# Kernel optimization log

Measured on AMD Instinct MI355X. Metric: run time of the kernel, lower is better.

## Reference

```python
import jax, jax.numpy as jnp
import numpy as np

LN_EPS = 1e-5

def _ln(x, g, b):
    mu = jnp.mean(x, axis=-1, keepdims=True)
    var = jnp.mean((x - mu) ** 2, axis=-1, keepdims=True)
    return (x - mu) * jax.lax.rsqrt(var + LN_EPS) * g + b

def _gelu(x):
    return jax.nn.gelu(x, approximate=False)

def _time_embed(t, dim):
    # standard sinusoidal embedding on scalar times t: (B,) -> (B, dim)
    half = dim // 2
    freqs = jnp.exp(-jnp.log(10000.0) * jnp.arange(half, dtype=jnp.float32) / max(half - 1, 1))
    ang = t[:, None] * freqs[None, :]
    return jnp.concatenate([jnp.sin(ang), jnp.cos(ang)], axis=-1)

def setup_inputs() -> dict:
    key = jax.random.key(0)
    B, D, C, H, M = 1024, 128, 256, 512, 64
    ks = jax.random.split(key, 24)
    w = lambda k, shp: jax.random.normal(k, shp, dtype=jnp.float32) * 0.02
    inp = {
        "noise": jax.random.normal(ks[0], (B, D), dtype=jnp.float32),
        "context": jax.random.normal(ks[1], (B, C), dtype=jnp.float32),
        "support_memory": jax.random.normal(ks[2], (B, M, D), dtype=jnp.float32),
        "num_steps": 4,
        # memory adapter: LayerNorm(D) + Linear(D->H)
        "mem_ln_g": jnp.ones((D,), jnp.float32), "mem_ln_b": jnp.zeros((D,), jnp.float32),
        "Wa": w(ks[3], (D, H)), "ba": jnp.zeros((H,), jnp.float32),
        # attention projections H->H
        "Wq": w(ks[4], (H, H)), "bq": jnp.zeros((H,), jnp.float32),
        "Wk": w(ks[5], (H, H)), "bk": jnp.zeros((H,), jnp.float32),
        "Wv": w(ks[6], (H, H)), "bv": jnp.zeros((H,), jnp.float32),
        "Wo": w(ks[7], (H, H)), "bo": jnp.zeros((H,), jnp.float32),
        # particle proj: LN(D) + Linear(D->H) + GELU + Linear(H->H)
        "pp_ln_g": jnp.ones((D,), jnp.float32), "pp_ln_b": jnp.zeros((D,), jnp.float32),
        "Wp1": w(ks[8], (D, H)), "bp1": jnp.zeros((H,), jnp.float32),
        "Wp2": w(ks[9], (H, H)), "bp2": jnp.zeros((H,), jnp.float32),
        # context proj C->H
        "Wc": w(ks[10], (C, H)), "bc": jnp.zeros((H,), jnp.float32),
        # time proj H->H (on sinusoidal embedding of dim H)
        "Wt": w(ks[11], (H, H)), "bt": jnp.zeros((H,), jnp.float32),
        # fusion head: LN(4H) + Linear(4H->H) + GELU + Linear(H->D)
        "f_ln_g": jnp.ones((4 * H,), jnp.float32), "f_ln_b": jnp.zeros((4 * H,), jnp.float32),
        "Wf1": w(ks[12], (4 * H, H)), "bf1": jnp.zeros((H,), jnp.float32),
        "Wf2": w(ks[13], (H, D)), "bf2": jnp.zeros((D,), jnp.float32),
    }
    return inp

def reference(noise, context, support_memory, num_steps,
              mem_ln_g, mem_ln_b, Wa, ba,
              Wq, bq, Wk, bk, Wv, bv, Wo, bo,
              pp_ln_g, pp_ln_b, Wp1, bp1, Wp2, bp2,
              Wc, bc, Wt, bt,
              f_ln_g, f_ln_b, Wf1, bf1, Wf2, bf2):
    B, D = noise.shape
    H = Wq.shape[0]
    heads = 4
    dh = H // heads
    scale = dh ** -0.5

    # encode support memory once (solver-invariant), like encode_memory()
    enc = _ln(support_memory, mem_ln_g, mem_ln_b) @ Wa + ba            # (B, M, H)
    M = enc.shape[1]
    k_mem = (enc @ Wk + bk).reshape(B, M, heads, dh)                    # (B, M, h, dh)
    v_mem = (enc @ Wv + bv).reshape(B, M, heads, dh)
    ctx_h = context @ Wc + bc                                           # (B, H)

    def velocity(y, t):
        te = _time_embed(t, H) @ Wt + bt                                # (B, H)
        h = _gelu(_ln(y, pp_ln_g, pp_ln_b) @ Wp1 + bp1) @ Wp2 + bp2      # (B, H)
        q = (h @ Wq + bq).reshape(B, heads, dh)
        logits = jnp.einsum('bhd,bmhd->bhm', q, k_mem) * scale
        attn = jax.nn.softmax(logits, axis=-1)
        summ = jnp.einsum('bhm,bmhd->bhd', attn, v_mem).reshape(B, H)
        m = summ @ Wo + bo                                              # (B, H)
        z = jnp.concatenate([h, m, ctx_h, te], axis=-1)                 # (B, 4H)
        return _gelu(_ln(z, f_ln_g, f_ln_b) @ Wf1 + bf1) @ Wf2 + bf2     # (B, D)

    dt = 1.0 / float(num_steps)
    t0s = jnp.arange(num_steps, dtype=jnp.float32) * dt

    def heun_step(y, t0):
        tb0 = jnp.full((B,), t0, dtype=y.dtype)
        k1 = velocity(y, tb0)
        k2 = velocity(y + dt * k1, tb0 + dt)
        return y + 0.5 * dt * (k1 + k2), None

    y_final, _ = jax.lax.scan(heun_step, noise, t0s)
    return y_final
```

## Files before the change

### kernel.cpp

```cpp
#include <hip/hip_runtime.h>
#include <hip/hip_bf16.h>
#include <cstdint>
#include <cstddef>

#define LN_EPS 1e-5f

typedef __attribute__((ext_vector_type(8))) short short8;
typedef __attribute__((ext_vector_type(4))) float f32x4;

__device__ __forceinline__ float gelu_exact(float x) {
  return 0.5f * x * (1.0f + erff(x * 0.70710678118654752440f));
}
__device__ __forceinline__ float bflo(unsigned int x) {
  union { unsigned int i; float f; } v; v.i = x << 16; return v.f;
}
__device__ __forceinline__ float bfhi(unsigned int x) {
  union { unsigned int i; float f; } v; v.i = x & 0xffff0000u; return v.f;
}
__device__ __forceinline__ float bf2f(short s) {
  union { unsigned int i; float f; } v; v.i = ((unsigned int)(unsigned short)s) << 16; return v.f;
}
__device__ __forceinline__ short bf16s(float f) {
  __hip_bfloat16 h = __float2bfloat16(f);
  return *reinterpret_cast<short*>(&h);
}

__global__ __launch_bounds__(256) void ln_bf16_k(const float* __restrict__ X,
                                                 const float* __restrict__ KIN, float a,
                                                 const float* __restrict__ g,
                                                 const float* __restrict__ bb,
                                                 __hip_bfloat16* __restrict__ out, int rows) {
  int row = blockIdx.x * 4 + (threadIdx.x >> 6);
  if (row >= rows) return;
  int l = threadIdx.x & 63;
  size_t base = (size_t)row * 128;
  float x0 = X[base + l], x1 = X[base + l + 64];
  if (KIN) { x0 += a * KIN[base + l]; x1 += a * KIN[base + l + 64]; }
  float s = x0 + x1;
#pragma unroll
  for (int o = 32; o > 0; o >>= 1) s += __shfl_xor(s, o);
  float mu = s * (1.0f / 128.0f);
  float d0 = x0 - mu, d1 = x1 - mu;
  float v = d0 * d0 + d1 * d1;
#pragma unroll
  for (int o = 32; o > 0; o >>= 1) v += __shfl_xor(v, o);
  float rstd = rsqrtf(v * (1.0f / 128.0f) + LN_EPS);
  out[base + l] = __float2bfloat16(d0 * rstd * g[l] + bb[l]);
  out[base + l + 64] = __float2bfloat16(d1 * rstd * g[l + 64] + bb[l + 64]);
}

template <int ROWS, int BN, bool GELU_OUT, bool OUT_BF16>
__global__ __launch_bounds__(ROWS * 4) void gemm_mfma_k(
    const short* __restrict__ A, const short* __restrict__ WT,
    const float* __restrict__ bias, void* __restrict__ Cout,
    int K, int lda, int ldw, int ldc, float alpha,
    int hsA, int hsB, long hsC) {
// ... 27 lines not shown
    for (int i = 0; i < NB; ++i) {
      int c = tid + i * T;
      bR[i] = *(const short8*)(WT + (size_t)(col0 + (c >> 3)) * ldw + k0 + (c & 7) * 8);
    }
  };
  auto storeT = [&](int buf) {
    int c1 = tid + T;
    *(short8*)&As[buf][tid >> 3][(tid & 7) * 8] = aR0;
    *(short8*)&As[buf][c1 >> 3][(c1 & 7) * 8] = aR1;
#pragma unroll
    for (int i = 0; i < NB; ++i) {
      int c = tid + i * T;
      *(short8*)&Bs[buf][c >> 3][(c & 7) * 8] = bR[i];
    }
  };

  loadA(0);
  loadB(0);
  for (int t = 0; t < nt; ++t) {
    int buf = t & 1;
    storeT(buf);
    __syncthreads();
    if (t + 1 < nt) { loadA(t + 1); loadB(t + 1); }
    short8 af0 = *(const short8*)&As[buf][w * 16 + (l & 15)][(l >> 4) * 8];
    short8 af1 = *(const short8*)&As[buf][w * 16 + (l & 15)][(l >> 4) * 8 + 32];
#pragma unroll
    for (int nc = 0; nc < NFRAG; ++nc) {
      short8 bf0 = *(const short8*)&Bs[buf][nc * 16 + (l & 15)][(l >> 4) * 8];
      acc[nc] = __builtin_amdgcn_mfma_f32_16x16x32_bf16(af0, bf0, acc[nc], 0, 0, 0);
      short8 bf1 = *(const short8*)&Bs[buf][nc * 16 + (l & 15)][(l >> 4) * 8 + 32];
      acc[nc] = __builtin_amdgcn_mfma_f32_16x16x32_bf16(af1, bf1, acc[nc], 0, 0, 0);
    }
    __syncthreads();
  }
  const int cr = (l >> 4) * 4;
  const int cc = l & 15;
#pragma unroll
  for (int nc = 0; nc < NFRAG; ++nc) {
    int gc = col0 + nc * 16 + cc;
    float bv = bias ? bias[gc] : 0.0f;
#pragma unroll
    for (int r = 0; r < 4; ++r) {
      int gr = row0 + w * 16 + cr + r;
      float v = acc[nc][r] * alpha + bv;
      if (GELU_OUT) v = gelu_exact(v);
      if (OUT_BF16)
        ((__hip_bfloat16*)Cout)[cOff + (size_t)gr * ldc + gc] = __float2bfloat16(v);
      else
        ((float*)Cout)[cOff + (size_t)gr * ldc + gc] = v;
    }
  }
}

__global__ __launch_bounds__(128) void zgemm2_k(
    const short* __restrict__ hq, const short* __restrict__ mo,
    const float* __restrict__ ctxWg, const float* __restrict__ teWgRow,
    const float* __restrict__ u, const float* __restrict__ cbv,
    const float* __restrict__ murs, const short* __restrict__ WgT,
    short* __restrict__ outC) {
  __shared__ __align__(16) short As[2][32][72];
  __shared__ __align__(16) short Bs[2][32][72];
  const int tid = threadIdx.x;
  const int w = tid >> 6, l = tid & 63;
  const int row0 = blockIdx.y * 32, col0 = blockIdx.x * 32;
  const int rA0 = tid >> 3, rA1 = rA0 + 16, kc = (tid & 7) * 8;
  f32x4 acc[2];
  acc[0] = (f32x4){0.f, 0.f, 0.f, 0.f};
  acc[1] = (f32x4){0.f, 0.f, 0.f, 0.f};
  short8 aR0, aR1;
  short8 bR[2];
  auto loadA = [&](int t) {
    const int k = t * 64 + kc;
    const short* src;
    int stride, koff;
    if (k < 512) { src = hq; stride = 1024; koff = k; }
    else         { src = mo; stride = 512;  koff = k - 512; }
    aR0 = *(const short8*)(src + (size_t)(row0 + rA0) * stride + koff);
    aR1 = *(const short8*)(src + (size_t)(row0 + rA1) * stride + koff);
  };
  auto loadB = [&](int t) {
    int k0 = t * 64;
#pragma unroll
    for (int i = 0; i < 2; ++i) {
      int c = tid + i * 128;
      bR[i] = *(const short8*)(WgT + (size_t)(col0 + (c >> 3)) * 2048 + k0 + (c & 7) * 8);
    }
  };
  auto storeT = [&](int buf) {
    *(short8*)&As[buf][rA0][kc] = aR0;
    *(short8*)&As[buf][rA1][kc] = aR1;
#pragma unroll
    for (int i = 0; i < 2; ++i) {
      int c = tid + i * 128;
      *(short8*)&Bs[buf][c >> 3][(c & 7) * 8] = bR[i];
    }
  };

  loadA(0);
  loadB(0);
  for (int t = 0; t < 16; ++t) {
    int buf = t & 1;
    storeT(buf);
    __syncthreads();
    if (t + 1 < 16) { loadA(t + 1); loadB(t + 1); }
    short8 af0 = *(const short8*)&As[buf][w * 16 + (l & 15)][(l >> 4) * 8];
    short8 af1 = *(const short8*)&As[buf][w * 16 + (l & 15)][(l >> 4) * 8 + 32];
#pragma unroll
    for (int nc = 0; nc < 2; ++nc) {
      short8 bf0 = *(const short8*)&Bs[buf][nc * 16 + (l & 15)][(l >> 4) * 8];
      acc[nc] = __builtin_amdgcn_mfma_f32_16x16x32_bf16(af0, bf0, acc[nc], 0, 0, 0);
      short8 bf1 = *(const short8*)&Bs[buf][nc * 16 + (l & 15)][(l >> 4) * 8 + 32];
      acc[nc] = __builtin_amdgcn_mfma_f32_16x16x32_bf16(af1, bf1, acc[nc], 0, 0, 0);
    }
    __syncthreads();
  }
  const int cr = (l >> 4) * 4, cc = l & 15;
#pragma unroll
  for (int nc = 0; nc < 2; ++nc) {
    int gc = col0 + nc * 16 + cc;
    float uu = u[gc], cb = cbv[gc], tw = teWgRow[gc];
#pragma unroll
    for (int r = 0; r < 4; ++r) {
      int gr = row0 + w * 16 + cr + r;
      float mu = murs[2 * gr], rs = murs[2 * gr + 1];
      float v = rs * (acc[nc][r] + ctxWg[(size_t)gr * 512 + gc] + tw - mu * uu) + cb;
      outC[(size_t)gr * 512 + gc] = bf16s(gelu_exact(v));
    }
  }
}

__global__ __launch_bounds__(256) void zstats_k(const short* __restrict__ hq,
                                                const short* __restrict__ mo,
                                                const float* __restrict__ ctxsums,
                                                const float* __restrict__ teSums2,
                                                float* __restrict__ murs, int rows) {
  int row = blockIdx.x * 4 + (threadIdx.x >> 6);
  if (row >= rows) return;
  int l = threadIdx.x & 63;
  short8 hv = *(const short8*)(hq + (size_t)row * 1024 + l * 8);
  short8 mv = *(const short8*)(mo + (size_t)row * 512 + l * 8);
  float s = 0.f, s2 = 0.f;
#pragma unroll
  for (int j = 0; j < 8; ++j) {
    float fa = bf2f(hv[j]), fb = bf2f(mv[j]);
    s += fa + fb;
    s2 += fa * fa + fb * fb;
  }
#pragma unroll
  for (int o = 32; o > 0; o >>= 1) { s += __shfl_xor(s, o); s2 += __shfl_xor(s2, o); }
  if (l == 0) {
    float S = s + ctxsums[2 * row] + teSums2[0];
    float S2 = s2 + ctxsums[2 * row + 1] + teSums2[1];
    float mu = S * (1.0f / 2048.0f);
    murs[2 * row] = mu;
    murs[2 * row + 1] = rsqrtf(S2 * (1.0f / 2048.0f) - mu * mu + LN_EPS);
  }
}

__global__ __launch_bounds__(256) void rowsum_k(const short* __restrict__ X,
                                                float* __restrict__ sums, int rows) {
  int row = blockIdx.x * 4 + (threadIdx.x >> 6);
  if (row >= rows) return;
  int l = threadIdx.x & 63;
  short8 v = *(const short8*)(X + (size_t)row * 512 + l * 8);
  float s = 0.f, s2 = 0.f;
#pragma unroll
  for (int j = 0; j < 8; ++j) { float f = bf2f(v[j]); s += f; s2 += f * f; }
#pragma unroll
  for (int o = 32; o > 0; o >>= 1) { s += __shfl_xor(s, o); s2 += __shfl_xor(s2, o); }
  if (l == 0) { sums[2 * row] = s; sums[2 * row + 1] = s2; }
}

__global__ __launch_bounds__(512) void vmp_k(const float* __restrict__ va,
                                             const float* __restrict__ vb,
                                             const float* __restrict__ W,
                                             int woff, int hsA,
                                             float* __restrict__ part) {
  const int j = threadIdx.x;
  const int b = blockIdx.x, z = blockIdx.z;
  const float* vaz = va + (size_t)z * hsA;
  float s = 0.f;
#pragma unroll 4
  for (int i = 0; i < 16; ++i) {
    int k = b * 16 + i;
    float c = vaz[k];
    if (vb) c *= vb[k];
    s += c * W[(size_t)(woff + k) * 512 + j];
  }
  part[((size_t)z * gridDim.x + b) * 512 + j] = s;
}

__global__ __launch_bounds__(512) void vmr_k(const float* __restrict__ part,
                                             const float* __restrict__ base, int KB,
                                             float* __restrict__ out, int hsOut) {
  const int j = threadIdx.x;
  const int z = blockIdx.z;
  float s = base ? base[j] : 0.f;
  for (int b = 0; b < KB; ++b) s += part[((size_t)z * KB + b) * 512 + j];
  out[(size_t)z * hsOut + j] = s;
}

__global__ __launch_bounds__(256) void transpose_cast_scale_k(
    const float* __restrict__ W, const float* __restrict__ scale,
    short* __restrict__ WT, int K, int N) {
  __shared__ float tile[64][65];
  int n0 = blockIdx.x * 64, k0 = blockIdx.y * 64;
#pragma unroll
  for (int i = 0; i < 16; ++i) {
    int e = threadIdx.x + i * 256;
    int r = e >> 6, c = e & 63;
    tile[r][c] = W[(size_t)(k0 + r) * N + n0 + c] * scale[k0 + r];
  }
  __syncthreads();
#pragma unroll
  for (int i = 0; i < 16; ++i) {
    int e = threadIdx.x + i * 256;
    int r = e >> 6, c = e & 63;
    WT[(size_t)(n0 + r) * K + k0 + c] = bf16s(tile[c][r]);
  }
}

__global__ __launch_bounds__(256) void gemm_heun_k(
    const short* __restrict__ A, const short* __restrict__ WT,
    const float* __restrict__ bias, const float* __restrict__ yin,
    const float* __restrict__ kaux, float c0, float* __restrict__ outY) {
  __shared__ __align__(16) short As[2][64][72];
  __shared__ __align__(16) short Bs[2][32][72];
  const int tid = threadIdx.x;
  const int w = tid >> 6, l = tid & 63;
  const int row0 = blockIdx.y * 64, col0 = blockIdx.x * 32;
  f32x4 acc[2];
  acc[0] = (f32x4){0.f, 0.f, 0.f, 0.f};
  acc[1] = (f32x4){0.f, 0.f, 0.f, 0.f};
  short8 aR0, aR1, bR;
  auto loadA = [&](int t) {
    int k0 = t * 64;
    int c1 = tid + 256;
    aR0 = *(const short8*)(A + (size_t)(row0 + (tid >> 3)) * 512 + k0 + (tid & 7) * 8);
    aR1 = *(const short8*)(A + (size_t)(row0 + (c1 >> 3)) * 512 + k0 + (c1 & 7) * 8);
  };
  auto loadB = [&](int t) {
    int k0 = t * 64;
    bR = *(const short8*)(WT + (size_t)(col0 + (tid >> 3)) * 512 + k0 + (tid & 7) * 8);
  };
  auto storeT = [&](int buf) {
    int c1 = tid + 256;
    *(short8*)&As[buf][tid >> 3][(tid & 7) * 8] = aR0;
    *(short8*)&As[buf][c1 >> 3][(c1 & 7) * 8] = aR1;
    *(short8*)&Bs[buf][tid >> 3][(tid & 7) * 8] = bR;
  };
  loadA(0);
  loadB(0);
  for (int t = 0; t < 8; ++t) {
    int buf = t & 1;
    storeT(buf);
    __syncthreads();
    if (t + 1 < 8) { loadA(t + 1); loadB(t + 1); }
    short8 af0 = *(const short8*)&As[buf][w * 16 + (l & 15)][(l >> 4) * 8];
    short8 af1 = *(const short8*)&As[buf][w * 16 + (l & 15)][(l >> 4) * 8 + 32];
#pragma unroll
    for (int nc = 0; nc < 2; ++nc) {
      short8 bf0 = *(const short8*)&Bs[buf][nc * 16 + (l & 15)][(l >> 4) * 8];
      acc[nc] = __builtin_amdgcn_mfma_f32_16x16x32_bf16(af0, bf0, acc[nc], 0, 0, 0);
      short8 bf1 = *(const short8*)&Bs[buf][nc * 16 + (l & 15)][(l >> 4) * 8 + 32];
      acc[nc] = __builtin_amdgcn_mfma_f32_16x16x32_bf16(af1, bf1, acc[nc], 0, 0, 0);
    }
    __syncthreads();
  }
  const int cr = (l >> 4) * 4, cc = l & 15;
#pragma unroll
  for (int nc = 0; nc < 2; ++nc) {
    int gc = col0 + nc * 16 + cc;
    float bv = bias[gc];
#pragma unroll
    for (int r = 0; r < 4; ++r) {
      int gr = row0 + w * 16 + cr + r;
      float v = acc[nc][r] + bv;
      size_t idx = (size_t)gr * 128 + gc;
      outY[idx] = yin[idx] + c0 * (kaux[idx] + v);
    }
  }
}

struct TCBatch { const float* src[5]; short* dst[5]; };
__global__ __launch_bounds__(256) void transpose_cast_batch_k(TCBatch p) {
  const float* W = p.src[blockIdx.z];
  short* WT = p.dst[blockIdx.z];
  __shared__ float tile[64][65];
  int n0 = blockIdx.x * 64, k0 = blockIdx.y * 64;
#pragma unroll
  for (int i = 0; i < 16; ++i) {
    int e = threadIdx.x + i * 256;
    int r = e >> 6, c = e & 63;
    tile[r][c] = W[(size_t)(k0 + r) * 512 + n0 + c];
  }
  __syncthreads();
#pragma unroll
  for (int i = 0; i < 16; ++i) {
    int e = threadIdx.x + i * 256;
    int r = e >> 6, c = e & 63;
    WT[(size_t)(n0 + r) * 512 + k0 + c] = bf16s(tile[c][r]);
  }
}

__global__ __launch_bounds__(256) void transpose_cast_k(const float* __restrict__ W,
                                                        short* __restrict__ WT,
                                                        int K, int N) {
  __shared__ float tile[64][65];
  int n0 = blockIdx.x * 64, k0 = blockIdx.y * 64;
#pragma unroll
  for (int i = 0; i < 16; ++i) {
    int e = threadIdx.x + i * 256;
    int r = e >> 6, c = e & 63;
    tile[r][c] = W[(size_t)(k0 + r) * N + n0 + c];
  }
  __syncthreads();
#pragma unroll
  for (int i = 0; i < 16; ++i) {
    int e = threadIdx.x + i * 256;
    int r = e >> 6, c = e & 63;
    WT[(size_t)(n0 + r) * K + k0 + c] = bf16s(tile[c][r]);
  }
}

__global__ void cast_bf16_k(const float* __restrict__ src, short* __restrict__ dst, int n) {
  int i = blockIdx.x * blockDim.x + threadIdx.x;
  if (i < n) dst[i] = bf16s(src[i]);
}

__global__ __launch_bounds__(256) void bqp_k(const float* __restrict__ bhqq,
                                             const short* __restrict__ Wak_bf,
                                             float scale, float* __restrict__ bqp) {
  const int tid = threadIdx.x;
  const int j = blockIdx.x * 32 + (tid >> 3);
  const int h = j >> 7, e = j & 127;
  const int kl = tid & 7;
  float s = 0.f;
  for (int d = kl; d < 128; d += 8)
    s += bhqq[h * 128 + d] * bf2f(Wak_bf[(size_t)e * 512 + h * 128 + d]);
  s += __shfl_xor(s, 1);
  s += __shfl_xor(s, 2);
  s += __shfl_xor(s, 4);
  if (kl == 0) bqp[j] = s * scale;
}

__global__ __launch_bounds__(512) void te_k(const float* __restrict__ Wt,
                                            const float* __restrict__ bt,
                                            float* __restrict__ te,
                                            float* __restrict__ teSums) {
  __shared__ float emb[512];
  __shared__ float red[8];
  const int ci = blockIdx.x;
  const float t = 0.25f * (float)((ci >> 1) + (ci & 1));
  const int j = threadIdx.x;
  if (j < 256) {
    float fr = expf(-9.210340371976184f * (float)j * (1.0f / 255.0f));
    float ang = t * fr;
    emb[j] = sinf(ang);
    emb[j + 256] = cosf(ang);
  }
  __syncthreads();
  float s0 = 0.f, s1 = 0.f, s2 = 0.f, s3 = 0.f;
  for (int k = 0; k < 512; k += 4) {
    s0 += emb[k] * Wt[(size_t)k * 512 + j];
    s1 += emb[k + 1] * Wt[(size_t)(k + 1) * 512 + j];
    s2 += emb[k + 2] * Wt[(size_t)(k + 2) * 512 + j];
    s3 += emb[k + 3] * Wt[(size_t)(k + 3) * 512 + j];
  }
  float val = bt[j] + ((s0 + s1) + (s2 + s3));
  te[(size_t)ci * 512 + j] = val;
  float sv = val, sq = val * val;
#pragma unroll
  for (int o = 32; o > 0; o >>= 1) { sv += __shfl_xor(sv, o); sq += __shfl_xor(sq, o); }
  if ((j & 63) == 0) red[j >> 6] = sv;
  __syncthreads();
  if (j == 0) {
    float tot = 0.f;
    for (int i = 0; i < 8; ++i) tot += red[i];
    teSums[2 * ci] = tot;
  }
  __syncthreads();
  if ((j & 63) == 0) red[j >> 6] = sq;
  __syncthreads();
  if (j == 0) {
    float tot = 0.f;
    for (int i = 0; i < 8; ++i) tot += red[i];
    teSums[2 * ci + 1] = tot;
  }
}

__global__ __launch_bounds__(256) void attn_k(const __hip_bfloat16* __restrict__ hq,
                                              const short* __restrict__ lnsm,
                                              __hip_bfloat16* __restrict__ sctx) {
  const int b = blockIdx.x;
  const int tid = threadIdx.x;
  const int w = tid >> 6, l = tid & 63;
  __shared__ __align__(16) short smt[64 * 128];
  __shared__ float qs[512];
  __shared__ float att[4][64];
  {
    unsigned int u = ((const unsigned int*)(hq + (size_t)b * 1024 + 512))[tid];
    qs[2 * tid] = bflo(u);
    qs[2 * tid + 1] = bfhi(u);
  }
  {
    const int m = tid >> 2;
    const short* src = lnsm + ((size_t)b * 64 + m) * 128;
#pragma unroll
    for (int j = 0; j < 4; ++j) {
      int c = (tid & 3) + 4 * j;
      short8 v = *(const short8*)(src + c * 8);
      *(short8*)&smt[m * 128 + ((c ^ (m & 7)) * 8)] = v;
    }
  }
  __syncthreads();
  const float* qh = qs + w * 128;
  float acc = 0.f;
#pragma unroll
  for (int i = 0; i < 16; ++i) {
    uint4 u = *(const uint4*)&smt[l * 128 + ((i ^ (l & 7)) * 8)];
    const int d = i * 8;
    acc += bflo(u.x) * qh[d + 0] + bfhi(u.x) * qh[d + 1] +
           bflo(u.y) * qh[d + 2] + bfhi(u.y) * qh[d + 3] +
           bflo(u.z) * qh[d + 4] + bfhi(u.z) * qh[d + 5] +
           bflo(u.w) * qh[d + 6] + bfhi(u.w) * qh[d + 7];
  }
  float mx = acc;
#pragma unroll
  for (int o = 32; o > 0; o >>= 1) mx = fmaxf(mx, __shfl_xor(mx, o));
  float e = expf(acc - mx);
  float se = e;
#pragma unroll
  for (int o = 32; o > 0; o >>= 1) se += __shfl_xor(se, o);
  att[w][l] = e / se;
  const int cb = l >> 2, doff = 2 * (l & 3);
  float a0 = 0.f, a1 = 0.f;
#pragma unroll 8
  for (int m = 0; m < 64; ++m) {
    float am = att[w][m];
    unsigned int u = *(const unsigned int*)&smt[m * 128 + ((cb ^ (m & 7)) * 8) + doff];
    a0 += am * bflo(u);
    a1 += am * bfhi(u);
  }
  unsigned int pr = ((unsigned int)(unsigned short)bf16s(a1) << 16) |
                    (unsigned int)(unsigned short)bf16s(a0);
  ((unsigned int*)(sctx + (size_t)b * 512 + w * 128))[l] = pr;
}

extern "C" void kernel_launch(void* const* d_in, const int* in_sizes, int n_in,
                              void* d_out, int out_size, void* d_ws, size_t ws_size,
                              hipStream_t stream) {
  (void)in_sizes; (void)n_in; (void)out_size; (void)ws_size;
  const int B = 1024, Mm = 64;
  const int BMrows = B * Mm;
  const float ATTN_SCALE = 0.08838834764831845f;
  const size_t SL = (size_t)512 * 512;

  const float* noise = (const float*)d_in[0];
  const float* context = (const float*)d_in[1];
  const float* sm = (const float*)d_in[2];
  const float* mem_ln_g = (const float*)d_in[4];
  const float* mem_ln_b = (const float*)d_in[5];
  const float* Wa = (const float*)d_in[6];
  const float* ba = (const float*)d_in[7];
  const float* Wq = (const float*)d_in[8];
  const float* bq = (const float*)d_in[9];
  const float* Wk = (const float*)d_in[10];
  const float* bk = (const float*)d_in[11];
  (void)bk;
  const float* Wv = (const float*)d_in[12];
  const float* bv = (const float*)d_in[13];
  const float* Wo = (const float*)d_in[14];
  const float* bo = (const float*)d_in[15];
  const float* pp_ln_g = (const float*)d_in[16];
  const float* pp_ln_b = (const float*)d_in[17];
  const float* Wp1 = (const float*)d_in[18];
  const float* bp1 = (const float*)d_in[19];
  const float* Wp2 = (const float*)d_in[20];
  const float* bp2 = (const float*)d_in[21];
  const float* Wc = (const float*)d_in[22];
  const float* bc = (const float*)d_in[23];
  const float* Wt = (const float*)d_in[24];
  const float* bt = (const float*)d_in[25];
  const float* f_ln_g = (const float*)d_in[26];
  const float* f_ln_b = (const float*)d_in[27];
  const float* Wf1 = (const float*)d_in[28];
  const float* bf1 = (const float*)d_in[29];
  const float* Wf2 = (const float*)d_in[30];
  const float* bf2 = (const float*)d_in[31];
  float* out = (float*)d_out;

  char* wsb = (char*)d_ws;
  size_t off = 0;
  auto alloc = [&](size_t bytes) -> void* {
    off = (off + 255) & ~(size_t)255;
    void* p = wsb + off;
    off += bytes;
    return p;
  };
// ... 35 lines not shown
  short* yln = (short*)alloc((size_t)B * 128 * 2);
  short* hmid = (short*)alloc((size_t)B * 512 * 2);
  short* hqbuf = (short*)alloc((size_t)B * 1024 * 2);
  short* sctx = (short*)alloc((size_t)B * 512 * 2);
  short* mobuf = (short*)alloc((size_t)B * 512 * 2);
  short* fmid = (short*)alloc((size_t)B * 512 * 2);

  ln_bf16_k<<<BMrows / 4, 256, 0, stream>>>(sm, nullptr, 0.f, mem_ln_g, mem_ln_b,
                                            (__hip_bfloat16*)lnsm, BMrows);
  cast_bf16_k<<<(128 * 512 + 255) / 256, 256, 0, stream>>>(Wa, WaB, 128 * 512);
  cast_bf16_k<<<(512 * 512 + 255) / 256, 256, 0, stream>>>(Wp2, Wp2B, 512 * 512);
  cast_bf16_k<<<(B * 256 + 255) / 256, 256, 0, stream>>>(context, ctxb, B * 256);
  {
    TCBatch p;
    p.src[0] = Wk; p.src[1] = Wv; p.src[2] = Wq; p.src[3] = Wo; p.src[4] = Wp2;
    p.dst[0] = WkT; p.dst[1] = WvT; p.dst[2] = WqT; p.dst[3] = WoT; p.dst[4] = WhqT;
    transpose_cast_batch_k<<<dim3(8, 8, 5), 256, 0, stream>>>(p);
  }
  transpose_cast_k<<<dim3(8, 2), 256, 0, stream>>>(Wp1, Wp1T, 128, 512);
  transpose_cast_k<<<dim3(8, 4), 256, 0, stream>>>(Wc, WcT, 256, 512);
  transpose_cast_scale_k<<<dim3(8, 32), 256, 0, stream>>>(Wf1, f_ln_g, WgT, 2048, 512);
  transpose_cast_k<<<dim3(2, 8), 256, 0, stream>>>(Wf2, Wf2T, 512, 128);
  gemm_mfma_k<64, 64, false, true><<<dim3(8, 2, 2), 256, 0, stream>>>(
      WaB, WkT, nullptr, WakavB, 512, 512, 512, 512, 1.f, 0, (int)SL, 128 * 512);
  gemm_mfma_k<64, 64, false, true><<<dim3(8, 8), 256, 0, stream>>>(
      Wp2B, WqT, nullptr, Wp2q_bf, 512, 512, 512, 512, 1.f, 0, 0, 0);
  gemm_mfma_k<64, 64, false, true><<<dim3(8, 2, 4), 256, 0, stream>>>(
      Wak_bf, Wp2q_bf, nullptr, WhqT + SL, 128, 512, 512, 512, ATTN_SCALE,
      128, 128, 128 * 512);
  gemm_mfma_k<64, 64, false, true><<<dim3(2, 8, 4), 256, 0, stream>>>(
      WoT, Wav_bf, nullptr, WfoldT, 128, 512, 512, 512, 1.f, 128, 128, 128);
  vmp_k<<<dim3(32, 1, 1), 512, 0, stream>>>(bp2, nullptr, Wq, 0, 0, vpart);
  vmr_k<<<dim3(1, 1, 1), 512, 0, stream>>>(vpart, bq, 32, bhqq, 512);
  bqp_k<<<16, 256, 0, stream>>>(bhqq, Wak_bf, ATTN_SCALE, bhq + 512);
  hipMemcpyAsync(bhq, bp2, 512 * 4, hipMemcpyDeviceToDevice, stream);
  vmp_k<<<dim3(32, 1, 1), 512, 0, stream>>>(ba, nullptr, Wv, 0, 0, vpart);
  vmr_k<<<dim3(1, 1, 1), 512, 0, stream>>>(vpart, bv, 32, bav, 512);
  vmp_k<<<dim3(32, 1, 1), 512, 0, stream>>>(bav, nullptr, Wo, 0, 0, vpart);
  vmr_k<<<dim3(1, 1, 1), 512, 0, stream>>>(vpart, bo, 32, bofold, 512);
  gemm_mfma_k<64, 64, false, true><<<dim3(8, 16), 256, 0, stream>>>(
      ctxb, WcT, bc, ctxh, 256, 256, 256, 512, 1.f, 0, 0, 0);
  te_k<<<8, 512, 0, stream>>>(Wt, bt, te_table, teSums);
  vmp_k<<<dim3(128, 1, 1), 512, 0, stream>>>(f_ln_g, nullptr, Wf1, 0, 0, vpart);
  vmr_k<<<dim3(1, 1, 1), 512, 0, stream>>>(vpart, nullptr, 128, uvec, 512);
  vmp_k<<<dim3(128, 1, 1), 512, 0, stream>>>(f_ln_b, nullptr, Wf1, 0, 0, vpart);
  vmr_k<<<dim3(1, 1, 1), 512, 0, stream>>>(vpart, bf1, 128, cbv, 512);
  vmp_k<<<dim3(32, 1, 8), 512, 0, stream>>>(te_table, f_ln_g + 1536, Wf1, 1536, 512, vpart);
  vmr_k<<<dim3(1, 1, 8), 512, 0, stream>>>(vpart, nullptr, 32, teWg, 512);
  gemm_mfma_k<64, 64, false, false><<<dim3(8, 16), 256, 0, stream>>>(
      ctxh, WgT + 1024, nullptr, ctxWg, 512, 512, 2048, 512, 1.f, 0, 0, 0);
  rowsum_k<<<B / 4, 256, 0, stream>>>(ctxh, ctxsums, B);

  const float dt = 0.25f;
  auto chain = [&](const float* ycur, const float* kin, float a, int tidx) {
    ln_bf16_k<<<B / 4, 256, 0, stream>>>(ycur, kin, a, pp_ln_g, pp_ln_b,
                                         (__hip_bfloat16*)yln, B);
    gemm_mfma_k<32, 32, true, true><<<dim3(16, 32), 128, 0, stream>>>(
        yln, Wp1T, bp1, hmid, 128, 128, 128, 512, 1.f, 0, 0, 0);
    gemm_mfma_k<32, 64, false, true><<<dim3(16, 32), 128, 0, stream>>>(
        hmid, WhqT, bhq, hqbuf, 512, 512, 512, 1024, 1.f, 0, 0, 0);
    attn_k<<<B, 256, 0, stream>>>((const __hip_bfloat16*)hqbuf, lnsm,
                                  (__hip_bfloat16*)sctx);
    gemm_mfma_k<32, 32, false, true><<<dim3(16, 32), 128, 0, stream>>>(
        sctx, WfoldT, bofold, mobuf, 512, 512, 512, 512, 1.f, 0, 0, 0);
    zstats_k<<<B / 4, 256, 0, stream>>>(hqbuf, mobuf, ctxsums, teSums + 2 * tidx,
                                        murs, B);
    zgemm2_k<<<dim3(16, 32), 128, 0, stream>>>(
        hqbuf, mobuf, ctxWg, teWg + (size_t)tidx * 512, uvec, cbv, murs, WgT, fmid);
  };

  const float* ycur = noise;
  for (int s = 0; s < 4; ++s) {
    chain(ycur, nullptr, 0.f, 2 * s);
    gemm_mfma_k<32, 32, false, false><<<dim3(4, 32), 128, 0, stream>>>(
        fmid, Wf2T, bf2, k1, 512, 512, 512, 128, 1.f, 0, 0, 0);
    chain(ycur, k1, dt, 2 * s + 1);
    float* ynext = (s == 3) ? out : ybuf;
    gemm_heun_k<<<dim3(4, 16), 256, 0, stream>>>(
        fmid, Wf2T, bf2, ycur, k1, 0.5f * dt, ynext);
    ycur = ybuf;
  }
}
```

Measured before the change: 587.2 us.

## Fuse per-velocity kernel chain into one cooperative persistent kernel with grid syncs

Replaces the sequence of about eight launches per velocity evaluation (LN, four GEMMs, attention, stats, fusion GEMM, output GEMM) with a single cooperative kernel of 256 blocks that moves between stages using grid.sync(). GEMM tiles become 64-row with 256 threads so each block maps to one tile per stage, and attention is handled as four batch rows per block. The aim is to remove launch overhead and inter-kernel gaps. In exchange, only 256 blocks of one wave-size run at a time, which may reduce occupancy and latency hiding, and each grid barrier has its own cost.

```diff
diff --git a/kernel.cpp b/kernel.cpp
--- a/kernel.cpp
+++ b/kernel.cpp
@@ -1,7 +1,10 @@
 #include <hip/hip_runtime.h>
 #include <hip/hip_bf16.h>
+#include <hip/hip_cooperative_groups.h>
 #include <cstdint>
 #include <cstddef>
+
+namespace cg = cooperative_groups;
 
 #define LN_EPS 1e-5f
 
@@ -135,23 +138,105 @@
   }
 }
 
-__global__ __launch_bounds__(128) void zgemm2_k(
+template <int BN, bool GELU_OUT, bool OUT_BF16, int EPI>
+__device__ __forceinline__ void dev_gemm64(
+    const short* __restrict__ A, const short* __restrict__ WT,
+    const float* __restrict__ bias, void* __restrict__ Cout,
+    int K, int lda, int ldw, int ldc, int tileX, int tileY, char* smem,
+    const float* __restrict__ yin, const float* __restrict__ kaux, float c0) {
+  constexpr int NFRAG = BN / 16;
+  constexpr int NB = (BN * 8) / 256;
+  short (*As)[64][72] = (short (*)[64][72])smem;
+  short (*Bs)[BN][72] = (short (*)[BN][72])(smem + 18432);
+  const int tid = threadIdx.x;
+  const int w = tid >> 6, l = tid & 63;
+  const int row0 = tileY * 64, col0 = tileX * BN;
+  f32x4 acc[NFRAG];
+#pragma unroll
+  for (int i = 0; i < NFRAG; ++i) acc[i] = (f32x4){0.f, 0.f, 0.f, 0.f};
+  const int nt = K >> 6;
+  short8 aR0, aR1;
+  short8 bR[NB];
+  auto loadA = [&](int t) {
+    int k0 = t * 64;
+    int c1 = tid + 256;
+    aR0 = *(const short8*)(A + (size_t)(row0 + (tid >> 3)) * lda + k0 + (tid & 7) * 8);
+    aR1 = *(const short8*)(A + (size_t)(row0 + (c1 >> 3)) * lda + k0 + (c1 & 7) * 8);
+  };
+  auto loadB = [&](int t) {
+    int k0 = t * 64;
+#pragma unroll
+    for (int i = 0; i < NB; ++i) {
+      int c = tid + i * 256;
+      bR[i] = *(const short8*)(WT + (size_t)(col0 + (c >> 3)) * ldw + k0 + (c & 7) * 8);
+    }
+  };
+  auto storeT = [&](int buf) {
+    int c1 = tid + 256;
+    *(short8*)&As[buf][tid >> 3][(tid & 7) * 8] = aR0;
+    *(short8*)&As[buf][c1 >> 3][(c1 & 7) * 8] = aR1;
+#pragma unroll
+    for (int i = 0; i < NB; ++i) {
+      int c = tid + i * 256;
+      *(short8*)&Bs[buf][c >> 3][(c & 7) * 8] = bR[i];
+    }
+  };
+  loadA(0);
+  loadB(0);
+  for (int t = 0; t < nt; ++t) {
+    int buf = t & 1;
+    storeT(buf);
+    __syncthreads();
+    if (t + 1 < nt) { loadA(t + 1); loadB(t + 1); }
+    short8 af0 = *(const short8*)&As[buf][w * 16 + (l & 15)][(l >> 4) * 8];
+    short8 af1 = *(const short8*)&As[buf][w * 16 + (l & 15)][(l >> 4) * 8 + 32];
+#pragma unroll
+    for (int nc = 0; nc < NFRAG; ++nc) {
+      short8 bf0 = *(const short8*)&Bs[buf][nc * 16 + (l & 15)][(l >> 4) * 8];
+      acc[nc] = __builtin_amdgcn_mfma_f32_16x16x32_bf16(af0, bf0, acc[nc], 0, 0, 0);
+      short8 bf1 = *(const short8*)&Bs[buf][nc * 16 + (l & 15)][(l >> 4) * 8 + 32];
+      acc[nc] = __builtin_amdgcn_mfma_f32_16x16x32_bf16(af1, bf1, acc[nc], 0, 0, 0);
+    }
+    __syncthreads();
+  }
+  const int cr = (l >> 4) * 4, cc = l & 15;
+#pragma unroll
+  for (int nc = 0; nc < NFRAG; ++nc) {
+    int gc = col0 + nc * 16 + cc;
+    float bv = bias ? bias[gc] : 0.0f;
+#pragma unroll
+    for (int r = 0; r < 4; ++r) {
+      int gr = row0 + w * 16 + cr + r;
+      float v = acc[nc][r] + bv;
+      if (GELU_OUT) v = gelu_exact(v);
+      size_t idx = (size_t)gr * ldc + gc;
+      if (EPI == 2) {
+        ((float*)Cout)[idx] = yin[idx] + c0 * (kaux[idx] + v);
+      } else if (OUT_BF16) {
+        ((__hip_bfloat16*)Cout)[idx] = __float2bfloat16(v);
+      } else {
+        ((float*)Cout)[idx] = v;
+      }
+    }
+  }
+}
+
+__device__ __forceinline__ void dev_zgemm64(
     const short* __restrict__ hq, const short* __restrict__ mo,
     const float* __restrict__ ctxWg, const float* __restrict__ teWgRow,
     const float* __restrict__ u, const float* __restrict__ cbv,
     const float* __restrict__ murs, const short* __restrict__ WgT,
-    short* __restrict__ outC) {
-  __shared__ __align__(16) short As[2][32][72];
-  __shared__ __align__(16) short Bs[2][32][72];
+    short* __restrict__ outC, int tileX, int tileY, char* smem) {
+  short (*As)[64][72] = (short (*)[64][72])smem;
+  short (*Bs)[32][72] = (short (*)[32][72])(smem + 18432);
   const int tid = threadIdx.x;
   const int w = tid >> 6, l = tid & 63;
-  const int row0 = blockIdx.y * 32, col0 = blockIdx.x * 32;
-  const int rA0 = tid >> 3, rA1 = rA0 + 16, kc = (tid & 7) * 8;
+  const int row0 = tileY * 64, col0 = tileX * 32;
+  const int rA0 = tid >> 3, rA1 = rA0 + 32, kc = (tid & 7) * 8;
   f32x4 acc[2];
   acc[0] = (f32x4){0.f, 0.f, 0.f, 0.f};
   acc[1] = (f32x4){0.f, 0.f, 0.f, 0.f};
-  short8 aR0, aR1;
-  short8 bR[2];
+  short8 aR0, aR1, bR;
   auto loadA = [&](int t) {
     const int k = t * 64 + kc;
     const short* src;
@@ -162,23 +247,13 @@
     aR1 = *(const short8*)(src + (size_t)(row0 + rA1) * stride + koff);
   };
   auto loadB = [&](int t) {
-    int k0 = t * 64;
-#pragma unroll
-    for (int i = 0; i < 2; ++i) {
-      int c = tid + i * 128;
-      bR[i] = *(const short8*)(WgT + (size_t)(col0 + (c >> 3)) * 2048 + k0 + (c & 7) * 8);
-    }
+    bR = *(const short8*)(WgT + (size_t)(col0 + (tid >> 3)) * 2048 + t * 64 + kc);
   };
   auto storeT = [&](int buf) {
     *(short8*)&As[buf][rA0][kc] = aR0;
     *(short8*)&As[buf][rA1][kc] = aR1;
-#pragma unroll
-    for (int i = 0; i < 2; ++i) {
-      int c = tid + i * 128;
-      *(short8*)&Bs[buf][c >> 3][(c & 7) * 8] = bR[i];
-    }
-  };
-
+    *(short8*)&Bs[buf][tid >> 3][kc] = bR;
+  };
   loadA(0);
   loadB(0);
   for (int t = 0; t < 16; ++t) {
@@ -212,46 +287,220 @@
   }
 }
 
-__global__ __launch_bounds__(256) void zstats_k(const short* __restrict__ hq,
-                                                const short* __restrict__ mo,
-                                                const float* __restrict__ ctxsums,
-                                                const float* __restrict__ teSums2,
-                                                float* __restrict__ murs, int rows) {
-  int row = blockIdx.x * 4 + (threadIdx.x >> 6);
-  if (row >= rows) return;
-  int l = threadIdx.x & 63;
-  short8 hv = *(const short8*)(hq + (size_t)row * 1024 + l * 8);
-  short8 mv = *(const short8*)(mo + (size_t)row * 512 + l * 8);
-  float s = 0.f, s2 = 0.f;
-#pragma unroll
-  for (int j = 0; j < 8; ++j) {
-    float fa = bf2f(hv[j]), fb = bf2f(mv[j]);
-    s += fa + fb;
-    s2 += fa * fa + fb * fb;
-  }
-#pragma unroll
-  for (int o = 32; o > 0; o >>= 1) { s += __shfl_xor(s, o); s2 += __shfl_xor(s2, o); }
-  if (l == 0) {
-    float S = s + ctxsums[2 * row] + teSums2[0];
-    float S2 = s2 + ctxsums[2 * row + 1] + teSums2[1];
-    float mu = S * (1.0f / 2048.0f);
-    murs[2 * row] = mu;
-    murs[2 * row + 1] = rsqrtf(S2 * (1.0f / 2048.0f) - mu * mu + LN_EPS);
-  }
-}
-
-__global__ __launch_bounds__(256) void rowsum_k(const short* __restrict__ X,
-                                                float* __restrict__ sums, int rows) {
-  int row = blockIdx.x * 4 + (threadIdx.x >> 6);
-  if (row >= rows) return;
-  int l = threadIdx.x & 63;
-  short8 v = *(const short8*)(X + (size_t)row * 512 + l * 8);
-  float s = 0.f, s2 = 0.f;
-#pragma unroll
-  for (int j = 0; j < 8; ++j) { float f = bf2f(v[j]); s += f; s2 += f * f; }
-#pragma unroll
-  for (int o = 32; o > 0; o >>= 1) { s += __shfl_xor(s, o); s2 += __shfl_xor(s2, o); }
-  if (l == 0) { sums[2 * row] = s; sums[2 * row + 1] = s2; }
+__device__ __forceinline__ void dev_attn(const __hip_bfloat16* __restrict__ hq,
+                                         const short* __restrict__ lnsm,
+                                         __hip_bfloat16* __restrict__ sctx,
+                                         int b, char* smem) {
+  short* smt = (short*)smem;
+  float* qs = (float*)(smem + 16384);
+  float (*att)[64] = (float (*)[64])(smem + 18432);
+  const int tid = threadIdx.x;
+  const int w = tid >> 6, l = tid & 63;
+  {
+    unsigned int u = ((const unsigned int*)(hq + (size_t)b * 1024 + 512))[tid];
+    qs[2 * tid] = bflo(u);
+    qs[2 * tid + 1] = bfhi(u);
+  }
+  {
+    const int m = tid >> 2;
+    const short* src = lnsm + ((size_t)b * 64 + m) * 128;
+#pragma unroll
+    for (int j = 0; j < 4; ++j) {
+      int c = (tid & 3) + 4 * j;
+      short8 v = *(const short8*)(src + c * 8);
+      *(short8*)&smt[m * 128 + ((c ^ (m & 7)) * 8)] = v;
+    }
+  }
+  __syncthreads();
+  const float* qh = qs + w * 128;
+  float acc = 0.f;
+#pragma unroll
+  for (int i = 0; i < 16; ++i) {
+    uint4 u = *(const uint4*)&smt[l * 128 + ((i ^ (l & 7)) * 8)];
+    const int d = i * 8;
+    acc += bflo(u.x) * qh[d + 0] + bfhi(u.x) * qh[d + 1] +
+           bflo(u.y) * qh[d + 2] + bfhi(u.y) * qh[d + 3] +
+           bflo(u.z) * qh[d + 4] + bfhi(u.z) * qh[d + 5] +
+           bflo(u.w) * qh[d + 6] + bfhi(u.w) * qh[d + 7];
+  }
+  float mx = acc;
+#pragma unroll
+  for (int o = 32; o > 0; o >>= 1) mx = fmaxf(mx, __shfl_xor(mx, o));
+  float e = expf(acc - mx);
+  float se = e;
+#pragma unroll
+  for (int o = 32; o > 0; o >>= 1) se += __shfl_xor(se, o);
+  att[w][l] = e / se;
+  const int cb = l >> 2, doff = 2 * (l & 3);
+  float a0 = 0.f, a1 = 0.f;
+#pragma unroll 8
+  for (int m = 0; m < 64; ++m) {
+    float am = att[w][m];
+    unsigned int u = *(const unsigned int*)&smt[m * 128 + ((cb ^ (m & 7)) * 8) + doff];
+    a0 += am * bflo(u);
+    a1 += am * bfhi(u);
+  }
+  unsigned int pr = ((unsigned int)(unsigned short)bf16s(a1) << 16) |
+                    (unsigned int)(unsigned short)bf16s(a0);
+  ((unsigned int*)(sctx + (size_t)b * 512 + w * 128))[l] = pr;
+}
+
+struct SolverArgs {
+  const float* ycur; const float* kin; float a;
+  const float* ppg; const float* ppb; short* yln;
+  const short* Wp1T; const float* bp1; short* hmid;
+  const short* WhqT; const float* bhq; short* hqbuf;
+  const short* lnsm; short* sctx;
+  const short* WfoldT; const float* bofold; short* mobuf;
+  const float* ctxsums; const float* teSums2; float* murs;
+  const short* WgT; const float* ctxWg; const float* teWgRow;
+  const float* uvec; const float* cbv; short* fmid;
+  const short* Wf2T; const float* bf2;
+  float* outY; const float* yin; const float* kaux; float c0;
+};
+
+template <int EPI>
+__global__ __launch_bounds__(256) void solver_k(SolverArgs p) {
+  __shared__ __align__(16) char smem[36864];
+  cg::grid_group grid = cg::this_grid();
+  const int blk = blockIdx.x;
+  const int tid = threadIdx.x;
+
+  {
+    int row = blk * 4 + (tid >> 6);
+    int l = tid & 63;
+    size_t base = (size_t)row * 128;
+    float x0 = p.ycur[base + l], x1 = p.ycur[base + l + 64];
+    if (EPI == 2) { x0 += p.a * p.kin[base + l]; x1 += p.a * p.kin[base + l + 64]; }
+    float s = x0 + x1;
+#pragma unroll
+    for (int o = 32; o > 0; o >>= 1) s += __shfl_xor(s, o);
+    float mu = s * (1.0f / 128.0f);
+    float d0 = x0 - mu, d1 = x1 - mu;
+    float v = d0 * d0 + d1 * d1;
+#pragma unroll
+    for (int o = 32; o > 0; o >>= 1) v += __shfl_xor(v, o);
+    float rstd = rsqrtf(v * (1.0f / 128.0f) + LN_EPS);
+    p.yln[base + l] = bf16s(d0 * rstd * p.ppg[l] + p.ppb[l]);
+    p.yln[base + l + 64] = bf16s(d1 * rstd * p.ppg[l + 64] + p.ppb[l + 64]);
+  }
+  grid.sync();
+  dev_gemm64<32, true, true, 0>(p.yln, p.Wp1T, p.bp1, p.hmid, 128, 128, 128, 512,
+                                blk & 15, blk >> 4, smem, nullptr, nullptr, 0.f);
+  grid.sync();
+  dev_gemm64<64, false, true, 0>(p.hmid, p.WhqT, p.bhq, p.hqbuf, 512, 512, 512, 1024,
+                                 blk & 15, blk >> 4, smem, nullptr, nullptr, 0.f);
+  grid.sync();
+  for (int i = 0; i < 4; ++i) {
+    dev_attn((const __hip_bfloat16*)p.hqbuf, p.lnsm, (__hip_bfloat16*)p.sctx,
+             blk * 4 + i, smem);
+    __syncthreads();
+  }
+  grid.sync();
+  dev_gemm64<32, false, true, 0>(p.sctx, p.WfoldT, p.bofold, p.mobuf, 512, 512, 512, 512,
+                                 blk & 15, blk >> 4, smem, nullptr, nullptr, 0.f);
+  grid.sync();
+  {
+    int row = blk * 4 + (tid >> 6);
+    int l = tid & 63;
+    short8 hv = *(const short8*)(p.hqbuf + (size_t)row * 1024 + l * 8);
+    short8 mv = *(const short8*)(p.mobuf + (size_t)row * 512 + l * 8);
+    float s = 0.f, s2 = 0.f;
+#pragma unroll
+    for (int j = 0; j < 8; ++j) {
+      float fa = bf2f(hv[j]), fb = bf2f(mv[j]);
+      s += fa + fb;
+      s2 += fa * fa + fb * fb;
+    }
+#pragma unroll
+    for (int o = 32; o > 0; o >>= 1) { s += __shfl_xor(s, o); s2 += __shfl_xor(s2, o); }
+    if (l == 0) {
+      float S = s + p.ctxsums[2 * row] + p.teSums2[0];
+      float S2 = s2 + p.ctxsums[2 * row + 1] + p.teSums2[1];
+      float mu = S * (1.0f / 2048.0f);
+      p.murs[2 * row] = mu;
+      p.murs[2 * row + 1] = rsqrtf(S2 * (1.0f / 2048.0f) - mu * mu + LN_EPS);
+    }
+  }
+  grid.sync();
+  dev_zgemm64(p.hqbuf, p.mobuf, p.ctxWg, p.teWgRow, p.uvec, p.cbv, p.murs, p.WgT,
+              p.fmid, blk & 15, blk >> 4, smem);
+  grid.sync();
+  if (blk < 64) {
+    if (EPI == 1) {
+      dev_gemm64<32, false, false, 0>(p.fmid, p.Wf2T, p.bf2, p.outY, 512, 512, 512, 128,
+                                      blk & 3, blk >> 2, smem, nullptr, nullptr, 0.f);
+    } else {
+      dev_gemm64<32, false, false, 2>(p.fmid, p.Wf2T, p.bf2, p.outY, 512, 512, 512, 128,
+                                      blk & 3, blk >> 2, smem, p.yin, p.kaux, p.c0);
+    }
+  }
+}
+
+struct TCBatch { const float* src[5]; short* dst[5]; };
+__global__ __launch_bounds__(256) void transpose_cast_batch_k(TCBatch p) {
+  const float* W = p.src[blockIdx.z];
+  short* WT = p.dst[blockIdx.z];
+  __shared__ float tile[64][65];
+  int n0 = blockIdx.x * 64, k0 = blockIdx.y * 64;
+#pragma unroll
+  for (int i = 0; i < 16; ++i) {
+    int e = threadIdx.x + i * 256;
+    int r = e >> 6, c = e & 63;
+    tile[r][c] = W[(size_t)(k0 + r) * 512 + n0 + c];
+  }
+  __syncthreads();
+#pragma unroll
+  for (int i = 0; i < 16; ++i) {
+    int e = threadIdx.x + i * 256;
+    int r = e >> 6, c = e & 63;
+    WT[(size_t)(n0 + r) * 512 + k0 + c] = bf16s(tile[c][r]);
+  }
+}
+
+__global__ __launch_bounds__(256) void transpose_cast_k(const float* __restrict__ W,
+                                                        short* __restrict__ WT,
+                                                        int K, int N) {
+  __shared__ float tile[64][65];
+  int n0 = blockIdx.x * 64, k0 = blockIdx.y * 64;
+#pragma unroll
+  for (int i = 0; i < 16; ++i) {
+    int e = threadIdx.x + i * 256;
+    int r = e >> 6, c = e & 63;
+    tile[r][c] = W[(size_t)(k0 + r) * N + n0 + c];
+  }
+  __syncthreads();
+#pragma unroll
+  for (int i = 0; i < 16; ++i) {
+    int e = threadIdx.x + i * 256;
+    int r = e >> 6, c = e & 63;
+    WT[(size_t)(n0 + r) * K + k0 + c] = bf16s(tile[c][r]);
+  }
+}
+
+__global__ __launch_bounds__(256) void transpose_cast_scale_k(
+    const float* __restrict__ W, const float* __restrict__ scale,
+    short* __restrict__ WT, int K, int N) {
+  __shared__ float tile[64][65];
+  int n0 = blockIdx.x * 64, k0 = blockIdx.y * 64;
+#pragma unroll
+  for (int i = 0; i < 16; ++i) {
+    int e = threadIdx.x + i * 256;
+    int r = e >> 6, c = e & 63;
+    tile[r][c] = W[(size_t)(k0 + r) * N + n0 + c] * scale[k0 + r];
+  }
+  __syncthreads();
+#pragma unroll
+  for (int i = 0; i < 16; ++i) {
+    int e = threadIdx.x + i * 256;
+    int r = e >> 6, c = e & 63;
+    WT[(size_t)(n0 + r) * K + k0 + c] = bf16s(tile[c][r]);
+  }
+}
+
+__global__ void cast_bf16_k(const float* __restrict__ src, short* __restrict__ dst, int n) {
+  int i = blockIdx.x * blockDim.x + threadIdx.x;
+  if (i < n) dst[i] = bf16s(src[i]);
 }
 
 __global__ __launch_bounds__(512) void vmp_k(const float* __restrict__ va,
@@ -283,134 +532,6 @@
   out[(size_t)z * hsOut + j] = s;
 }
 
-__global__ __launch_bounds__(256) void transpose_cast_scale_k(
-    const float* __restrict__ W, const float* __restrict__ scale,
-    short* __restrict__ WT, int K, int N) {
-  __shared__ float tile[64][65];
-  int n0 = blockIdx.x * 64, k0 = blockIdx.y * 64;
-#pragma unroll
-  for (int i = 0; i < 16; ++i) {
-    int e = threadIdx.x + i * 256;
-    int r = e >> 6, c = e & 63;
-    tile[r][c] = W[(size_t)(k0 + r) * N + n0 + c] * scale[k0 + r];
-  }
-  __syncthreads();
-#pragma unroll
-  for (int i = 0; i < 16; ++i) {
-    int e = threadIdx.x + i * 256;
-    int r = e >> 6, c = e & 63;
-    WT[(size_t)(n0 + r) * K + k0 + c] = bf16s(tile[c][r]);
-  }
-}
-
-__global__ __launch_bounds__(256) void gemm_heun_k(
-    const short* __restrict__ A, const short* __restrict__ WT,
-    const float* __restrict__ bias, const float* __restrict__ yin,
-    const float* __restrict__ kaux, float c0, float* __restrict__ outY) {
-  __shared__ __align__(16) short As[2][64][72];
-  __shared__ __align__(16) short Bs[2][32][72];
-  const int tid = threadIdx.x;
-  const int w = tid >> 6, l = tid & 63;
-  const int row0 = blockIdx.y * 64, col0 = blockIdx.x * 32;
-  f32x4 acc[2];
-  acc[0] = (f32x4){0.f, 0.f, 0.f, 0.f};
-  acc[1] = (f32x4){0.f, 0.f, 0.f, 0.f};
-  short8 aR0, aR1, bR;
-  auto loadA = [&](int t) {
-    int k0 = t * 64;
-    int c1 = tid + 256;
-    aR0 = *(const short8*)(A + (size_t)(row0 + (tid >> 3)) * 512 + k0 + (tid & 7) * 8);
-    aR1 = *(const short8*)(A + (size_t)(row0 + (c1 >> 3)) * 512 + k0 + (c1 & 7) * 8);
-  };
-  auto loadB = [&](int t) {
-    int k0 = t * 64;
-    bR = *(const short8*)(WT + (size_t)(col0 + (tid >> 3)) * 512 + k0 + (tid & 7) * 8);
-  };
-  auto storeT = [&](int buf) {
-    int c1 = tid + 256;
-    *(short8*)&As[buf][tid >> 3][(tid & 7) * 8] = aR0;
-    *(short8*)&As[buf][c1 >> 3][(c1 & 7) * 8] = aR1;
-    *(short8*)&Bs[buf][tid >> 3][(tid & 7) * 8] = bR;
-  };
-  loadA(0);
-  loadB(0);
-  for (int t = 0; t < 8; ++t) {
-    int buf = t & 1;
-    storeT(buf);
-    __syncthreads();
-    if (t + 1 < 8) { loadA(t + 1); loadB(t + 1); }
-    short8 af0 = *(const short8*)&As[buf][w * 16 + (l & 15)][(l >> 4) * 8];
-    short8 af1 = *(const short8*)&As[buf][w * 16 + (l & 15)][(l >> 4) * 8 + 32];
-#pragma unroll
-    for (int nc = 0; nc < 2; ++nc) {
-      short8 bf0 = *(const short8*)&Bs[buf][nc * 16 + (l & 15)][(l >> 4) * 8];
-      acc[nc] = __builtin_amdgcn_mfma_f32_16x16x32_bf16(af0, bf0, acc[nc], 0, 0, 0);
-      short8 bf1 = *(const short8*)&Bs[buf][nc * 16 + (l & 15)][(l >> 4) * 8 + 32];
-      acc[nc] = __builtin_amdgcn_mfma_f32_16x16x32_bf16(af1, bf1, acc[nc], 0, 0, 0);
-    }
-    __syncthreads();
-  }
-  const int cr = (l >> 4) * 4, cc = l & 15;
-#pragma unroll
-  for (int nc = 0; nc < 2; ++nc) {
-    int gc = col0 + nc * 16 + cc;
-    float bv = bias[gc];
-#pragma unroll
-    for (int r = 0; r < 4; ++r) {
-      int gr = row0 + w * 16 + cr + r;
-      float v = acc[nc][r] + bv;
-      size_t idx = (size_t)gr * 128 + gc;
-      outY[idx] = yin[idx] + c0 * (kaux[idx] + v);
-    }
-  }
-}
-
-struct TCBatch { const float* src[5]; short* dst[5]; };
-__global__ __launch_bounds__(256) void transpose_cast_batch_k(TCBatch p) {
-  const float* W = p.src[blockIdx.z];
-  short* WT = p.dst[blockIdx.z];
-  __shared__ float tile[64][65];
-  int n0 = blockIdx.x * 64, k0 = blockIdx.y * 64;
-#pragma unroll
-  for (int i = 0; i < 16; ++i) {
-    int e = threadIdx.x + i * 256;
-    int r = e >> 6, c = e & 63;
-    tile[r][c] = W[(size_t)(k0 + r) * 512 + n0 + c];
-  }
-  __syncthreads();
-#pragma unroll
-  for (int i = 0; i < 16; ++i) {
-    int e = threadIdx.x + i * 256;
-    int r = e >> 6, c = e & 63;
-    WT[(size_t)(n0 + r) * 512 + k0 + c] = bf16s(tile[c][r]);
-  }
-}
-
-__global__ __launch_bounds__(256) void transpose_cast_k(const float* __restrict__ W,
-                                                        short* __restrict__ WT,
-                                                        int K, int N) {
-  __shared__ float tile[64][65];
-  int n0 = blockIdx.x * 64, k0 = blockIdx.y * 64;
-#pragma unroll
-  for (int i = 0; i < 16; ++i) {
-    int e = threadIdx.x + i * 256;
-    int r = e >> 6, c = e & 63;
-    tile[r][c] = W[(size_t)(k0 + r) * N + n0 + c];
-  }
-  __syncthreads();
-#pragma unroll
-  for (int i = 0; i < 16; ++i) {
-    int e = threadIdx.x + i * 256;
-    int r = e >> 6, c = e & 63;
-    WT[(size_t)(n0 + r) * K + k0 + c] = bf16s(tile[c][r]);
-  }
-}
-
-__global__ void cast_bf16_k(const float* __restrict__ src, short* __restrict__ dst, int n) {
-  int i = blockIdx.x * blockDim.x + threadIdx.x;
-  if (i < n) dst[i] = bf16s(src[i]);
-}
-
 __global__ __launch_bounds__(256) void bqp_k(const float* __restrict__ bhqq,
                                              const short* __restrict__ Wak_bf,
                                              float scale, float* __restrict__ bqp) {
@@ -472,62 +593,18 @@
   }
 }
 
-__global__ __launch_bounds__(256) void attn_k(const __hip_bfloat16* __restrict__ hq,
-                                              const short* __restrict__ lnsm,
-                                              __hip_bfloat16* __restrict__ sctx) {
-  const int b = blockIdx.x;
-  const int tid = threadIdx.x;
-  const int w = tid >> 6, l = tid & 63;
-  __shared__ __align__(16) short smt[64 * 128];
-  __shared__ float qs[512];
-  __shared__ float att[4][64];
-  {
-    unsigned int u = ((const unsigned int*)(hq + (size_t)b * 1024 + 512))[tid];
-    qs[2 * tid] = bflo(u);
-    qs[2 * tid + 1] = bfhi(u);
-  }
-  {
-    const int m = tid >> 2;
-    const short* src = lnsm + ((size_t)b * 64 + m) * 128;
-#pragma unroll
-    for (int j = 0; j < 4; ++j) {
-      int c = (tid & 3) + 4 * j;
-      short8 v = *(const short8*)(src + c * 8);
-      *(short8*)&smt[m * 128 + ((c ^ (m & 7)) * 8)] = v;
-    }
-  }
-  __syncthreads();
-  const float* qh = qs + w * 128;
-  float acc = 0.f;
-#pragma unroll
-  for (int i = 0; i < 16; ++i) {
-    uint4 u = *(const uint4*)&smt[l * 128 + ((i ^ (l & 7)) * 8)];
-    const int d = i * 8;
-    acc += bflo(u.x) * qh[d + 0] + bfhi(u.x) * qh[d + 1] +
-           bflo(u.y) * qh[d + 2] + bfhi(u.y) * qh[d + 3] +
-           bflo(u.z) * qh[d + 4] + bfhi(u.z) * qh[d + 5] +
-           bflo(u.w) * qh[d + 6] + bfhi(u.w) * qh[d + 7];
-  }
-  float mx = acc;
-#pragma unroll
-  for (int o = 32; o > 0; o >>= 1) mx = fmaxf(mx, __shfl_xor(mx, o));
-  float e = expf(acc - mx);
-  float se = e;
-#pragma unroll
-  for (int o = 32; o > 0; o >>= 1) se += __shfl_xor(se, o);
-  att[w][l] = e / se;
-  const int cb = l >> 2, doff = 2 * (l & 3);
-  float a0 = 0.f, a1 = 0.f;
-#pragma unroll 8
-  for (int m = 0; m < 64; ++m) {
-    float am = att[w][m];
-    unsigned int u = *(const unsigned int*)&smt[m * 128 + ((cb ^ (m & 7)) * 8) + doff];
-    a0 += am * bflo(u);
-    a1 += am * bfhi(u);
-  }
-  unsigned int pr = ((unsigned int)(unsigned short)bf16s(a1) << 16) |
-                    (unsigned int)(unsigned short)bf16s(a0);
-  ((unsigned int*)(sctx + (size_t)b * 512 + w * 128))[l] = pr;
+__global__ __launch_bounds__(256) void rowsum_k(const short* __restrict__ X,
+                                                float* __restrict__ sums, int rows) {
+  int row = blockIdx.x * 4 + (threadIdx.x >> 6);
+  if (row >= rows) return;
+  int l = threadIdx.x & 63;
+  short8 v = *(const short8*)(X + (size_t)row * 512 + l * 8);
+  float s = 0.f, s2 = 0.f;
+#pragma unroll
+  for (int j = 0; j < 8; ++j) { float f = bf2f(v[j]); s += f; s2 += f * f; }
+#pragma unroll
+  for (int o = 32; o > 0; o >>= 1) { s += __shfl_xor(s, o); s2 += __shfl_xor(s2, o); }
+  if (l == 0) { sums[2 * row] = s; sums[2 * row + 1] = s2; }
 }
 
 extern "C" void kernel_launch(void* const* d_in, const int* in_sizes, int n_in,
@@ -669,32 +746,43 @@
   rowsum_k<<<B / 4, 256, 0, stream>>>(ctxh, ctxsums, B);
 
   const float dt = 0.25f;
-  auto chain = [&](const float* ycur, const float* kin, float a, int tidx) {
-    ln_bf16_k<<<B / 4, 256, 0, stream>>>(ycur, kin, a, pp_ln_g, pp_ln_b,
-                                         (__hip_bfloat16*)yln, B);
-    gemm_mfma_k<32, 32, true, true><<<dim3(16, 32), 128, 0, stream>>>(
-        yln, Wp1T, bp1, hmid, 128, 128, 128, 512, 1.f, 0, 0, 0);
-    gemm_mfma_k<32, 64, false, true><<<dim3(16, 32), 128, 0, stream>>>(
-        hmid, WhqT, bhq, hqbuf, 512, 512, 512, 1024, 1.f, 0, 0, 0);
-    attn_k<<<B, 256, 0, stream>>>((const __hip_bfloat16*)hqbuf, lnsm,
-                                  (__hip_bfloat16*)sctx);
-    gemm_mfma_k<32, 32, false, true><<<dim3(16, 32), 128, 0, stream>>>(
-        sctx, WfoldT, bofold, mobuf, 512, 512, 512, 512, 1.f, 0, 0, 0);
-    zstats_k<<<B / 4, 256, 0, stream>>>(hqbuf, mobuf, ctxsums, teSums + 2 * tidx,
-                                        murs, B);
-    zgemm2_k<<<dim3(16, 32), 128, 0, stream>>>(
-        hqbuf, mobuf, ctxWg, teWg + (size_t)tidx * 512, uvec, cbv, murs, WgT, fmid);
-  };
-
   const float* ycur = noise;
   for (int s = 0; s < 4; ++s) {
-    chain(ycur, nullptr, 0.f, 2 * s);
-    gemm_mfma_k<32, 32, false, false><<<dim3(4, 32), 128, 0, stream>>>(
-        fmid, Wf2T, bf2, k1, 512, 512, 512, 128, 1.f, 0, 0, 0);
-    chain(ycur, k1, dt, 2 * s + 1);
-    float* ynext = (s == 3) ? out : ybuf;
-    gemm_heun_k<<<dim3(4, 16), 256, 0, stream>>>(
-        fmid, Wf2T, bf2, ycur, k1, 0.5f * dt, ynext);
+    {
+      SolverArgs a;
+      a.ycur = ycur; a.kin = nullptr; a.a = 0.f;
+      a.ppg = pp_ln_g; a.ppb = pp_ln_b; a.yln = yln;
+      a.Wp1T = Wp1T; a.bp1 = bp1; a.hmid = hmid;
+      a.WhqT = WhqT; a.bhq = bhq; a.hqbuf = hqbuf;
+      a.lnsm = lnsm; a.sctx = sctx;
+      a.WfoldT = WfoldT; a.bofold = bofold; a.mobuf = mobuf;
+      a.ctxsums = ctxsums; a.teSums2 = teSums + 2 * (2 * s); a.murs = murs;
+      a.WgT = WgT; a.ctxWg = ctxWg; a.teWgRow = teWg + (size_t)(2 * s) * 512;
+      a.uvec = uvec; a.cbv = cbv; a.fmid = fmid;
+      a.Wf2T = Wf2T; a.bf2 = bf2;
+      a.outY = k1; a.yin = nullptr; a.kaux = nullptr; a.c0 = 0.f;
+      void* params[] = {&a};
+      hipLaunchCooperativeKernel((void*)solver_k<1>, dim3(256), dim3(256),
+                                 params, 0, stream);
+    }
+    {
+      float* ynext = (s == 3) ? out : ybuf;
+      SolverArgs a;
+      a.ycur = ycur; a.kin = k1; a.a = dt;
+      a.ppg = pp_ln_g; a.ppb = pp_ln_b; a.yln = yln;
+      a.Wp1T = Wp1T; a.bp1 = bp1; a.hmid = hmid;
+      a.WhqT = WhqT; a.bhq = bhq; a.hqbuf = hqbuf;
+      a.lnsm = lnsm; a.sctx = sctx;
+      a.WfoldT = WfoldT; a.bofold = bofold; a.mobuf = mobuf;
+      a.ctxsums = ctxsums; a.teSums2 = teSums + 2 * (2 * s + 1); a.murs = murs;
+      a.WgT = WgT; a.ctxWg = ctxWg; a.teWgRow = teWg + (size_t)(2 * s + 1) * 512;
+      a.uvec = uvec; a.cbv = cbv; a.fmid = fmid;
+      a.Wf2T = Wf2T; a.bf2 = bf2;
+      a.outY = ynext; a.yin = ycur; a.kaux = k1; a.c0 = 0.5f * dt;
+      void* params[] = {&a};
+      hipLaunchCooperativeKernel((void*)solver_k<2>, dim3(256), dim3(256),
+                                 params, 0, stream);
+    }
     ycur = ybuf;
   }
 }
```

Result: slower. 2.261 ms (+285.0%).
